# Optimization experiments

Hardware: AMD Instinct MI355X
Metric: run time of the kernel (lower is better)

Reference implementation:

```python
import jax, jax.numpy as jnp
import numpy as np

B, LQ, LKV = 4, 512, 4096
IN_DIM, N_HEADS, DIM_HEAD = 1024, 16, 64
INNER = N_HEADS * DIM_HEAD


def setup_inputs() -> dict:
    key = jax.random.key(0)
    ks = jax.random.split(key, 6)
    q = jax.random.normal(ks[0], (B, LQ, IN_DIM), dtype=jnp.float32)
    kv = jax.random.normal(ks[1], (B, LKV, IN_DIM), dtype=jnp.float32)
    mask = jax.random.randint(ks[2], (B, 1, 1, LKV), 0, 2).astype(jnp.bool_)
    w_scale = 0.02
    Wq = jax.random.normal(ks[3], (IN_DIM, INNER), dtype=jnp.float32) * w_scale
    Wkv = jax.random.normal(ks[4], (IN_DIM, 2 * INNER), dtype=jnp.float32) * w_scale
    Wo = jax.random.normal(ks[5], (INNER, IN_DIM), dtype=jnp.float32) * w_scale
    return {"q": q, "kv": kv, "mask": mask, "Wq": Wq, "Wkv": Wkv, "Wo": Wo}


def reference(q, kv, mask, Wq, Wkv, Wo):
    # projections
    qp = q @ Wq                                  # [B, LQ, INNER]
    kvp = kv @ Wkv                               # [B, LKV, 2*INNER]
    # split heads
    qh = qp.reshape(B, LQ, N_HEADS, DIM_HEAD).transpose(0, 2, 1, 3)   # [B,H,LQ,D]
    kvh = kvp.reshape(B, LKV, N_HEADS, 2 * DIM_HEAD).transpose(0, 2, 1, 3)
    kh, vh = kvh[..., :DIM_HEAD], kvh[..., DIM_HEAD:]                 # [B,H,LKV,D]
    scale = jnp.sqrt(jnp.asarray(DIM_HEAD, dtype=qh.dtype))
    scores = jnp.einsum("bhqd,bhkd->bhqk", qh, kh) / scale            # [B,H,LQ,LKV]
    scores = jnp.where(mask, -jnp.inf, scores)
    weights = jax.nn.softmax(scores, axis=-1)
    context = jnp.einsum("bhqk,bhkd->bhqd", weights, vh)              # [B,H,LQ,D]
    context = context.transpose(0, 2, 1, 3).reshape(B, LQ, INNER)
    return context @ Wo                                               # [B,LQ,IN_DIM]
```

## Files before the change

### kernel.cpp

```cpp
#include <hip/hip_runtime.h>
#include <hip/hip_bf16.h>
#include <math.h>

#define B_      4
#define LQ_     512
#define LKV_    4096
#define IN_DIM_ 1024
#define NH_     16
#define DH_     64
#define INNER_  1024

typedef _Float16 f16x8 __attribute__((ext_vector_type(8)));
typedef _Float16 f16x4 __attribute__((ext_vector_type(4)));
typedef float    f32x4 __attribute__((ext_vector_type(4)));

#define GLDS(gp, lp) __builtin_amdgcn_global_load_lds( \
    (const __attribute__((address_space(1))) void*)(gp), \
    (__attribute__((address_space(3))) void*)(lp), 16, 0, 0)

__global__ __launch_bounds__(256) void scan_mask(const int* __restrict__ mask,
                                                 int* __restrict__ pidx,
                                                 int* __restrict__ cnt) {
  __shared__ int wsum_s[4];
  int b = blockIdx.x, tid = threadIdx.x;
  const int* mb = mask + b * LKV_;
  int base = tid * 16;
  int vals[16];
#pragma unroll
  for (int i = 0; i < 4; ++i) {
    int4 v = *(const int4*)(mb + base + i * 4);
    vals[i * 4 + 0] = v.x; vals[i * 4 + 1] = v.y;
    vals[i * 4 + 2] = v.z; vals[i * 4 + 3] = v.w;
  }
  int s = 0;
#pragma unroll
  for (int j = 0; j < 16; ++j) s += (vals[j] == 0);
  int lane = tid & 63, wave = tid >> 6;
  int inc = s;
#pragma unroll
  for (int d = 1; d < 64; d <<= 1) {
    int v = __shfl_up(inc, d);
    if (lane >= d) inc += v;
  }
  if (lane == 63) wsum_s[wave] = inc;
  __syncthreads();
  int woff = 0;
#pragma unroll
  for (int w = 0; w < 4; ++w)
    if (w < wave) woff += wsum_s[w];
  if (tid == 255) cnt[b] = woff + inc;
  int run = woff + inc - s;
#pragma unroll
  for (int i = 0; i < 4; ++i) {
    int4 o;
    int* op = &o.x;
#pragma unroll
    for (int j = 0; j < 4; ++j) { op[j] = run; run += (vals[i * 4 + j] == 0); }
    *(int4*)(pidx + b * LKV_ + base + i * 4) = o;
  }
}

__device__ __forceinline__ void transpose_tile(const float* __restrict__ in,
                                               _Float16* __restrict__ out,
                                               int K, int N, int xb, int yb,
                                               float (*t)[33]) {
  int bn = xb * 32, bk = yb * 32;
  int tx = threadIdx.x & 31, ty = threadIdx.x >> 5;
#pragma unroll
  for (int i = 0; i < 4; ++i) {
    int r = ty + i * 8;
    t[r][tx] = in[(size_t)(bk + r) * N + bn + tx];
  }
  __syncthreads();
#pragma unroll
  for (int i = 0; i < 4; ++i) {
    int r = ty + i * 8;
    out[(size_t)(bn + r) * K + bk + tx] = (_Float16)t[tx][r];
  }
}

__global__ __launch_bounds__(256) void prep_compact(
    const float* __restrict__ kv, const float* __restrict__ q,
    const float* __restrict__ Wq, const float* __restrict__ Wkv,
    const float* __restrict__ Wo, const int* __restrict__ mask,
    const int* __restrict__ pidx,
    _Float16* __restrict__ kv16, _Float16* __restrict__ q16,
    _Float16* __restrict__ Wqt, _Float16* __restrict__ Wkvt,
    _Float16* __restrict__ Wot) {
  __shared__ float t[32][33];
  const int id = blockIdx.x, tid = threadIdx.x;
  if (id < 16384) {
    if (mask[id] != 0) return;
    int b = id >> 12;
    int dst = b * LKV_ + pidx[id];
    float4 v = ((const float4*)(kv + (size_t)id * IN_DIM_))[tid];
    f16x4 h = {(_Float16)v.x, (_Float16)v.y, (_Float16)v.z, (_Float16)v.w};
    ((f16x4*)(kv16 + (size_t)dst * IN_DIM_))[tid] = h;
  } else if (id < 18432) {
    int i = (id - 16384) * 256 + tid;
    float4 v = ((const float4*)q)[i];
    f16x4 h = {(_Float16)v.x, (_Float16)v.y, (_Float16)v.z, (_Float16)v.w};
    ((f16x4*)q16)[i] = h;
  } else if (id < 19456) {
    int l = id - 18432;
    transpose_tile(Wq, Wqt, 1024, 1024, l & 31, l >> 5, t);
  } else if (id < 21504) {
    int l = id - 19456;
    transpose_tile(Wkv, Wkvt, 1024, 2048, l & 63, l >> 6, t);
  } else {
    int l = id - 21504;
    transpose_tile(Wo, Wot, 1024, 1024, l & 31, l >> 5, t);
  }
}

__global__ __launch_bounds__(256, 2) void proj_f16(
    const _Float16* __restrict__ kv16, const _Float16* __restrict__ Wkvt,
    const _Float16* __restrict__ q16, const _Float16* __restrict__ Wqt,
    _Float16* __restrict__ qp16, _Float16* __restrict__ Kp,
    _Float16* __restrict__ Vt, const int* __restrict__ Cnt) {
  const int id = blockIdx.x;
  const bool is_kv = (id < 2048);
  int brow, bcol;
  const _Float16 *Ab, *Bb;
  if (is_kv) {
    bcol = (id & 15) * 128;
    brow = (id >> 4) * 128;
    if ((brow & 4095) >= Cnt[brow >> 12]) return;
    Ab = kv16 + (size_t)brow * 1024;
    Bb = Wkvt + (size_t)bcol * 1024;
  } else {
    int l = id - 2048;
    bcol = (l & 7) * 128;
    brow = (l >> 3) * 128;
    Ab = q16 + (size_t)brow * 1024;
    Bb = Wqt + (size_t)bcol * 1024;
  }
  __shared__ _Float16 As[128 * 128];
  __shared__ _Float16 Bs[128 * 128];
  const int tid = threadIdx.x;
  const int wave = tid >> 6, lane = tid & 63;
  const int quad = lane >> 4, l16 = lane & 15;
  const int wm = (wave & 1) * 64, wn = (wave >> 1) * 64;
  const int r4 = lane >> 4, ch = lane & 15;

  f32x4 acc[4][4];
#pragma unroll
  for (int i = 0; i < 4; ++i)
#pragma unroll
    for (int j = 0; j < 4; ++j) acc[i][j] = (f32x4){0.f, 0.f, 0.f, 0.f};

  for (int k0 = 0; k0 < 1024; k0 += 128) {
    __syncthreads();
#pragma unroll
    for (int i = 0; i < 8; ++i) {
      int rbase = wave * 32 + i * 4;
      int row = rbase + r4;
      int g = ch ^ (row & 15);
      GLDS(Ab + (size_t)row * 1024 + k0 + g * 8, &As[rbase * 128]);
      GLDS(Bb + (size_t)row * 1024 + k0 + g * 8, &Bs[rbase * 128]);
    }
    __syncthreads();
#pragma unroll
    for (int ks = 0; ks < 4; ++ks) {
      f16x8 af[4], bf[4];
      int c = ks * 4 + quad;
#pragma unroll
      for (int mt = 0; mt < 4; ++mt) {
        int r = wm + mt * 16 + l16;
        af[mt] = *(const f16x8*)&As[r * 128 + ((c ^ (r & 15)) * 8)];
        int rb = wn + mt * 16 + l16;
        bf[mt] = *(const f16x8*)&Bs[rb * 128 + ((c ^ (rb & 15)) * 8)];
      }
#pragma unroll
      for (int mt = 0; mt < 4; ++mt)
#pragma unroll
        for (int nt = 0; nt < 4; ++nt)
          acc[mt][nt] = __builtin_amdgcn_mfma_f32_16x16x32_f16(af[mt], bf[nt], acc[mt][nt], 0, 0, 0);
    }
  }

#pragma unroll
  for (int mt = 0; mt < 4; ++mt) {
    int row0 = brow + wm + mt * 16 + quad * 4;
#pragma unroll
    for (int nt = 0; nt < 4; ++nt) {
      int col = bcol + wn + nt * 16 + l16;
      f32x4 v = acc[mt][nt];
      if (is_kv) {
        int h = col >> 7, w64 = col & 63;
        if ((col & 127) < 64) {
#pragma unroll
          for (int r = 0; r < 4; ++r)
            Kp[(size_t)(row0 + r) * INNER_ + h * 64 + w64] = (_Float16)v[r];
        } else {
          int b = row0 >> 12, key = row0 & 4095;
          f16x4 pk = {(_Float16)v[0], (_Float16)v[1], (_Float16)v[2], (_Float16)v[3]};
          *(f16x4*)&Vt[((size_t)((b * NH_ + h) * DH_) + w64) * LKV_ + key] = pk;
        }
      } else {
#pragma unroll
        for (int r = 0; r < 4; ++r)
          qp16[(size_t)(row0 + r) * 1024 + col] = (_Float16)v[r];
      }
    }
  }
}

__global__ __launch_bounds__(256, 2) void attn_f16(
    const _Float16* __restrict__ qp, const _Float16* __restrict__ Kp,
    const _Float16* __restrict__ Vt, const int* __restrict__ cnt,
    float* __restrict__ opart, float* __restrict__ lpart) {
  const int idx = blockIdx.x;
  const int bh = idx & 63, qt = (idx >> 6) & 7, half = idx >> 9;
  const int b = bh >> 4, h = bh & 15;
  __shared__ _Float16 Ks[128 * 64];
  __shared__ _Float16 Vts[64 * 128];
  __shared__ _Float16 Pl[64][136];

  const int tid = threadIdx.x;
  const int wave = tid >> 6, lane = tid & 63;
  const int quad = lane >> 4, l16 = lane & 15;
  const int ro8 = lane >> 3, gch8 = (lane & 7) ^ (ro8 & 7);
  const int ro16 = lane >> 4, ch16 = lane & 15;

  const int qrow = b * LQ_ + qt * 64 + wave * 16 + l16;
  const _Float16* qpr = qp + (size_t)qrow * INNER_ + h * DH_;
  f16x8 qf[2];
  qf[0] = *(const f16x8*)(qpr + quad * 8);
  qf[1] = *(const f16x8*)(qpr + 32 + quad * 8);

  const int c_act = cnt[b];
  const int tiles = (c_act + 127) >> 7;
  const int htiles = (tiles + 1) >> 1;
  const int t0 = half * htiles;
  const int t1 = (half == 0) ? htiles : tiles;

  float l_run = 0.f;
  f32x4 oacc[4];
#pragma unroll
  for (int i = 0; i < 4; ++i) oacc[i] = (f32x4){0.f, 0.f, 0.f, 0.f};

  const _Float16* kb = Kp + (size_t)(b * LKV_) * INNER_ + h * DH_;
  const _Float16* vb = Vt + (size_t)((b * NH_ + h) * DH_) * LKV_;

  for (int t = t0; t < t1; ++t) {
    __syncthreads();
#pragma unroll
    for (int i = 0; i < 4; ++i) {
      int rbase = wave * 32 + i * 8;
      GLDS(kb + (size_t)(t * 128 + rbase + ro8) * INNER_ + gch8 * 8, &Ks[rbase * 64]);
    }
#pragma unroll
    for (int i = 0; i < 4; ++i) {
      int rbase = wave * 16 + i * 4;
      int row = rbase + ro16;
      int gch = ch16 ^ (row & 15);
      GLDS(vb + (size_t)row * LKV_ + t * 128 + gch * 8, &Vts[rbase * 128]);
    }
    __syncthreads();

    f32x4 sacc[8];
#pragma unroll
    for (int i = 0; i < 8; ++i) sacc[i] = (f32x4){0.f, 0.f, 0.f, 0.f};
#pragma unroll
    for (int ks = 0; ks < 2; ++ks) {
      int c = ks * 4 + quad;
#pragma unroll
      for (int mt = 0; mt < 8; ++mt) {
        int krow = mt * 16 + l16;
        f16x8 af = *(const f16x8*)&Ks[krow * 64 + ((c ^ (krow & 7)) * 8)];
        sacc[mt] = __builtin_amdgcn_mfma_f32_16x16x32_f16(af, qf[ks], sacc[mt], 0, 0, 0);
      }
    }
    const int lim = c_act - t * 128;
    float psloc = 0.f;
#pragma unroll
    for (int mt = 0; mt < 8; ++mt) {
      f16x4 pk;
#pragma unroll
      for (int r = 0; r < 4; ++r) {
        int key = mt * 16 + quad * 4 + r;
        float s = sacc[mt][r] * 0.125f;
        if (key >= lim) s = -1e30f;
        float p = __expf(s - 8.0f);
        psloc += p;
        pk[r] = (_Float16)p;
      }
      *(f16x4*)&Pl[wave * 16 + l16][mt * 16 + quad * 4] = pk;
    }
    psloc += __shfl_xor(psloc, 16);
    psloc += __shfl_xor(psloc, 32);
    l_run += psloc;
#pragma unroll
    for (int ks = 0; ks < 4; ++ks) {
      int c = ks * 4 + quad;
      f16x8 bf = *(const f16x8*)&Pl[wave * 16 + l16][ks * 32 + quad * 8];
#pragma unroll
      for (int mt = 0; mt < 4; ++mt) {
        int drow = mt * 16 + l16;
        f16x8 af = *(const f16x8*)&Vts[drow * 128 + ((c ^ (drow & 15)) * 8)];
        oacc[mt] = __builtin_amdgcn_mfma_f32_16x16x32_f16(af, bf, oacc[mt], 0, 0, 0);
      }
    }
  }

  float* ob = opart + ((size_t)(half * 2048 + qrow)) * INNER_ + h * DH_;
#pragma unroll
  for (int mt = 0; mt < 4; ++mt)
    *(f32x4*)(ob + mt * 16 + quad * 4) = oacc[mt];
  if (quad == 0) lpart[(size_t)(half * 2048 + qrow) * NH_ + h] = l_run;
}

__global__ __launch_bounds__(256) void attn_fin(const float* __restrict__ opart,
                                                const float* __restrict__ lpart,
                                                _Float16* __restrict__ ctx) {
  int row = blockIdx.x, t = threadIdx.x;
  int h = t >> 4;
  float l = lpart[(size_t)row * NH_ + h] + lpart[(size_t)(2048 + row) * NH_ + h];
  float inv = (l > 0.f) ? 1.f / l : 0.f;
  f32x4 a = *(const f32x4*)(opart + (size_t)row * INNER_ + t * 4);
  f32x4 c = *(const f32x4*)(opart + (size_t)(2048 + row) * INNER_ + t * 4);
  f16x4 o;
#pragma unroll
  for (int r = 0; r < 4; ++r) o[r] = (_Float16)((a[r] + c[r]) * inv);
  *(f16x4*)(ctx + (size_t)row * INNER_ + t * 4) = o;
}

__global__ __launch_bounds__(256, 2) void gemm_out(
    const _Float16* __restrict__ A, const _Float16* __restrict__ Bt,
    float* __restrict__ C) {
  const int brow = blockIdx.y * 64, bcol = blockIdx.x * 128;
  __shared__ _Float16 As[64 * 128];
  __shared__ _Float16 Bs[128 * 128];
  const int tid = threadIdx.x;
  const int wave = tid >> 6, lane = tid & 63;
  const int quad = lane >> 4, l16 = lane & 15;
  const int wm = (wave & 1) * 32, wn = (wave >> 1) * 64;
  const int r4 = lane >> 4, ch = lane & 15;

  f32x4 acc[2][4];
#pragma unroll
  for (int i = 0; i < 2; ++i)
#pragma unroll
    for (int j = 0; j < 4; ++j) acc[i][j] = (f32x4){0.f, 0.f, 0.f, 0.f};

  const _Float16* Ab = A + (size_t)brow * 1024;
  const _Float16* Bb = Bt + (size_t)bcol * 1024;

  for (int k0 = 0; k0 < 1024; k0 += 128) {
    __syncthreads();
#pragma unroll
    for (int i = 0; i < 4; ++i) {
      int rbase = wave * 16 + i * 4;
      int row = rbase + r4;
      int g = ch ^ (row & 15);
      GLDS(Ab + (size_t)row * 1024 + k0 + g * 8, &As[rbase * 128]);
    }
#pragma unroll
    for (int i = 0; i < 8; ++i) {
      int rbase = wave * 32 + i * 4;
      int row = rbase + r4;
      int g = ch ^ (row & 15);
      GLDS(Bb + (size_t)row * 1024 + k0 + g * 8, &Bs[rbase * 128]);
    }
    __syncthreads();
#pragma unroll
    for (int ks = 0; ks < 4; ++ks) {
      f16x8 af[2], bf[4];
      int c = ks * 4 + quad;
#pragma unroll
      for (int mt = 0; mt < 2; ++mt) {
        int r = wm + mt * 16 + l16;
        af[mt] = *(const f16x8*)&As[r * 128 + ((c ^ (r & 15)) * 8)];
      }
#pragma unroll
      for (int nt = 0; nt < 4; ++nt) {
        int rb = wn + nt * 16 + l16;
        bf[nt] = *(const f16x8*)&Bs[rb * 128 + ((c ^ (rb & 15)) * 8)];
      }
#pragma unroll
      for (int mt = 0; mt < 2; ++mt)
#pragma unroll
        for (int nt = 0; nt < 4; ++nt)
          acc[mt][nt] = __builtin_amdgcn_mfma_f32_16x16x32_f16(af[mt], bf[nt], acc[mt][nt], 0, 0, 0);
    }
  }

#pragma unroll
  for (int mt = 0; mt < 2; ++mt) {
    int row0 = brow + wm + mt * 16 + quad * 4;
#pragma unroll
    for (int nt = 0; nt < 4; ++nt) {
      int col = bcol + wn + nt * 16 + l16;
      f32x4 v = acc[mt][nt];
#pragma unroll
      for (int r = 0; r < 4; ++r) C[(size_t)(row0 + r) * 1024 + col] = v[r];
    }
  }
}

extern "C" void kernel_launch(void* const* d_in, const int* in_sizes, int n_in,
                              void* d_out, int out_size, void* d_ws, size_t ws_size,
                              hipStream_t stream) {
  const float* q   = (const float*)d_in[0];
  const float* kv  = (const float*)d_in[1];
  const int* mask  = (const int*)d_in[2];
  const float* Wq  = (const float*)d_in[3];
  const float* Wkv = (const float*)d_in[4];
  const float* Wo  = (const float*)d_in[5];
  float* out = (float*)d_out;

  _Float16* p = (_Float16*)d_ws;
  _Float16* q16   = p; p += (size_t)2048 * 1024;
  _Float16* kv16  = p; p += (size_t)16384 * 1024;
  _Float16* Wqt   = p; p += (size_t)1024 * 1024;
  _Float16* Wkvt  = p; p += (size_t)2048 * 1024;
  _Float16* Wot   = p; p += (size_t)1024 * 1024;
  _Float16* qp16  = p; p += (size_t)2048 * 1024;
  _Float16* Kp    = p; p += (size_t)16384 * 1024;
  _Float16* Vt    = p; p += (size_t)16384 * 1024;
  _Float16* ctx16 = p; p += (size_t)2048 * 1024;
  float* opart = (float*)p; p += (size_t)2 * 4096 * 1024;
  float* lpart = (float*)p; p += (size_t)2 * 2048 * NH_ * 2;
  int* pidx = (int*)p;
  int* cnt  = pidx + 16384;

  scan_mask<<<4, 256, 0, stream>>>(mask, pidx, cnt);
  prep_compact<<<22528, 256, 0, stream>>>(kv, q, Wq, Wkv, Wo, mask, pidx,
                                          kv16, q16, Wqt, Wkvt, Wot);
  proj_f16<<<2176, 256, 0, stream>>>(kv16, Wkvt, q16, Wqt, qp16, Kp, Vt, cnt);
  attn_f16<<<1024, 256, 0, stream>>>(qp16, Kp, Vt, cnt, opart, lpart);
  attn_fin<<<2048, 256, 0, stream>>>(opart, lpart, ctx16);
  gemm_out<<<dim3(8, 32), 256, 0, stream>>>(ctx16, Wot, out);
}
```

Before: 232.6 us.

## Double-buffer projection GEMM K-tiles and fuse attention finalize into output GEMM

The projection GEMM now splits K into 64-wide tiles held in two LDS buffers, issuing the next tile's async global-to-LDS loads before computing on the current one, with one barrier per step. The separate attention-finalize kernel is removed: the output GEMM now reads the two fp32 partial outputs and row sums, normalises them and converts to fp16 while filling its A tile. This removes one launch and the ctx intermediate round trip, at the cost of redundant partial reads across column blocks and synchronous loads inside the output GEMM loop.

```diff
diff --git a/kernel.cpp b/kernel.cpp
--- a/kernel.cpp
+++ b/kernel.cpp
@@ -135,13 +135,13 @@
     Ab = q16 + (size_t)brow * 1024;
     Bb = Wqt + (size_t)bcol * 1024;
   }
-  __shared__ _Float16 As[128 * 128];
-  __shared__ _Float16 Bs[128 * 128];
+  __shared__ _Float16 As[2][128 * 64];
+  __shared__ _Float16 Bs[2][128 * 64];
   const int tid = threadIdx.x;
   const int wave = tid >> 6, lane = tid & 63;
   const int quad = lane >> 4, l16 = lane & 15;
   const int wm = (wave & 1) * 64, wn = (wave >> 1) * 64;
-  const int r4 = lane >> 4, ch = lane & 15;
+  const int ro = lane >> 3, gch = (lane & 7) ^ ro;
 
   f32x4 acc[4][4];
 #pragma unroll
@@ -149,27 +149,38 @@
 #pragma unroll
     for (int j = 0; j < 4; ++j) acc[i][j] = (f32x4){0.f, 0.f, 0.f, 0.f};
 
-  for (int k0 = 0; k0 < 1024; k0 += 128) {
+#define PROJ_ISSUE(T)                                                        \
+  {                                                                          \
+    _Float16* as_ = As[(T) & 1];                                             \
+    _Float16* bs_ = Bs[(T) & 1];                                             \
+    const int k0_ = (T) * 64;                                                \
+    _Pragma("unroll")                                                        \
+    for (int i_ = 0; i_ < 4; ++i_) {                                         \
+      int rbase_ = wave * 32 + i_ * 8;                                       \
+      GLDS(Ab + (size_t)(rbase_ + ro) * 1024 + k0_ + gch * 8,                \
+           &as_[rbase_ * 64]);                                               \
+      GLDS(Bb + (size_t)(rbase_ + ro) * 1024 + k0_ + gch * 8,                \
+           &bs_[rbase_ * 64]);                                               \
+    }                                                                        \
+  }
+
+  PROJ_ISSUE(0);
+#pragma unroll
+  for (int t = 0; t < 16; ++t) {
     __syncthreads();
-#pragma unroll
-    for (int i = 0; i < 8; ++i) {
-      int rbase = wave * 32 + i * 4;
-      int row = rbase + r4;
-      int g = ch ^ (row & 15);
-      GLDS(Ab + (size_t)row * 1024 + k0 + g * 8, &As[rbase * 128]);
-      GLDS(Bb + (size_t)row * 1024 + k0 + g * 8, &Bs[rbase * 128]);
-    }
-    __syncthreads();
-#pragma unroll
-    for (int ks = 0; ks < 4; ++ks) {
+    if (t < 15) PROJ_ISSUE(t + 1);
+    const _Float16* as = As[t & 1];
+    const _Float16* bs = Bs[t & 1];
+#pragma unroll
+    for (int ks = 0; ks < 2; ++ks) {
       f16x8 af[4], bf[4];
       int c = ks * 4 + quad;
 #pragma unroll
       for (int mt = 0; mt < 4; ++mt) {
         int r = wm + mt * 16 + l16;
-        af[mt] = *(const f16x8*)&As[r * 128 + ((c ^ (r & 15)) * 8)];
+        af[mt] = *(const f16x8*)&as[r * 64 + ((c ^ (r & 7)) * 8)];
         int rb = wn + mt * 16 + l16;
-        bf[mt] = *(const f16x8*)&Bs[rb * 128 + ((c ^ (rb & 15)) * 8)];
+        bf[mt] = *(const f16x8*)&bs[rb * 64 + ((c ^ (rb & 7)) * 8)];
       }
 #pragma unroll
       for (int mt = 0; mt < 4; ++mt)
@@ -178,6 +189,7 @@
           acc[mt][nt] = __builtin_amdgcn_mfma_f32_16x16x32_f16(af[mt], bf[nt], acc[mt][nt], 0, 0, 0);
     }
   }
+#undef PROJ_ISSUE
 
 #pragma unroll
   for (int mt = 0; mt < 4; ++mt) {
@@ -311,24 +323,9 @@
   if (quad == 0) lpart[(size_t)(half * 2048 + qrow) * NH_ + h] = l_run;
 }
 
-__global__ __launch_bounds__(256) void attn_fin(const float* __restrict__ opart,
-                                                const float* __restrict__ lpart,
-                                                _Float16* __restrict__ ctx) {
-  int row = blockIdx.x, t = threadIdx.x;
-  int h = t >> 4;
-  float l = lpart[(size_t)row * NH_ + h] + lpart[(size_t)(2048 + row) * NH_ + h];
-  float inv = (l > 0.f) ? 1.f / l : 0.f;
-  f32x4 a = *(const f32x4*)(opart + (size_t)row * INNER_ + t * 4);
-  f32x4 c = *(const f32x4*)(opart + (size_t)(2048 + row) * INNER_ + t * 4);
-  f16x4 o;
-#pragma unroll
-  for (int r = 0; r < 4; ++r) o[r] = (_Float16)((a[r] + c[r]) * inv);
-  *(f16x4*)(ctx + (size_t)row * INNER_ + t * 4) = o;
-}
-
 __global__ __launch_bounds__(256, 2) void gemm_out(
-    const _Float16* __restrict__ A, const _Float16* __restrict__ Bt,
-    float* __restrict__ C) {
+    const float* __restrict__ opart, const float* __restrict__ lpart,
+    const _Float16* __restrict__ Bt, float* __restrict__ C) {
   const int brow = blockIdx.y * 64, bcol = blockIdx.x * 128;
   __shared__ _Float16 As[64 * 128];
   __shared__ _Float16 Bs[128 * 128];
@@ -344,24 +341,36 @@
 #pragma unroll
     for (int j = 0; j < 4; ++j) acc[i][j] = (f32x4){0.f, 0.f, 0.f, 0.f};
 
-  const _Float16* Ab = A + (size_t)brow * 1024;
   const _Float16* Bb = Bt + (size_t)bcol * 1024;
 
   for (int k0 = 0; k0 < 1024; k0 += 128) {
     __syncthreads();
-#pragma unroll
-    for (int i = 0; i < 4; ++i) {
-      int rbase = wave * 16 + i * 4;
-      int row = rbase + r4;
-      int g = ch ^ (row & 15);
-      GLDS(Ab + (size_t)row * 1024 + k0 + g * 8, &As[rbase * 128]);
-    }
 #pragma unroll
     for (int i = 0; i < 8; ++i) {
       int rbase = wave * 32 + i * 4;
       int row = rbase + r4;
       int g = ch ^ (row & 15);
       GLDS(Bb + (size_t)row * 1024 + k0 + g * 8, &Bs[rbase * 128]);
+    }
+#pragma unroll
+    for (int i = 0; i < 4; ++i) {
+      int cidx = tid + i * 256;
+      int row = cidx >> 4, sl = cidx & 15;
+      int g = sl ^ (row & 15);
+      int grow = brow + row;
+      const float* p0 = opart + (size_t)grow * 1024 + k0 + g * 8;
+      const float* p1 = p0 + (size_t)2048 * 1024;
+      f32x4 a0 = *(const f32x4*)p0, a1 = *(const f32x4*)(p0 + 4);
+      f32x4 b0 = *(const f32x4*)p1, b1 = *(const f32x4*)(p1 + 4);
+      int h = (k0 + g * 8) >> 6;
+      float l = lpart[(size_t)grow * NH_ + h] + lpart[(size_t)(2048 + grow) * NH_ + h];
+      float inv = (l > 0.f) ? 1.f / l : 0.f;
+      f16x8 o;
+#pragma unroll
+      for (int j = 0; j < 4; ++j) o[j] = (_Float16)((a0[j] + b0[j]) * inv);
+#pragma unroll
+      for (int j = 0; j < 4; ++j) o[4 + j] = (_Float16)((a1[j] + b1[j]) * inv);
+      *(f16x8*)&As[row * 128 + sl * 8] = o;
     }
     __syncthreads();
 #pragma unroll
@@ -430,6 +439,5 @@
                                           kv16, q16, Wqt, Wkvt, Wot);
   proj_f16<<<2176, 256, 0, stream>>>(kv16, Wkvt, q16, Wqt, qp16, Kp, Vt, cnt);
   attn_f16<<<1024, 256, 0, stream>>>(qp16, Kp, Vt, cnt, opart, lpart);
-  attn_fin<<<2048, 256, 0, stream>>>(opart, lpart, ctx16);
-  gemm_out<<<dim3(8, 32), 256, 0, stream>>>(ctx16, Wot, out);
-}
+  gemm_out<<<dim3(8, 32), 256, 0, stream>>>(opart, lpart, Wot, out);
+}
```

Result: slower. 252.8 us (+8.7%).
